# Optimization experiments

Hardware: AMD Instinct MI355X
Metric: run time of the kernel (lower is better)

The kernel has to match this reference:

```python
import jax, jax.numpy as jnp
import numpy as np

V = 32000   # vocab_size
S = 4096    # seq_len
D = 1024    # dim
H = 4096    # hidden_dim
L = 2       # num_layers
CS = 64     # chunk_size
R = 256     # low_rank_dim = max(8, D//4)
WIN = 8     # window_size (OptitationLayer default)
NEG = -1e30


def setup_inputs() -> dict:
    key = jax.random.key(0)
    ks = jax.random.split(key, 20)
    f32 = jnp.float32
    inp = {}
    inp['idx_seq'] = jax.random.randint(ks[0], (S,), 0, V)
    inp['embeddings'] = jax.random.normal(ks[1], (V, D), f32) * 0.01
    inp['positional'] = jax.random.normal(ks[2], (S, D), f32) * 0.01
    # per-layer MLP params, stacked over layer axis
    inp['Wg'] = jax.random.normal(ks[3], (L, D, D), f32) / D ** 0.5
    inp['bg'] = jnp.zeros((L, D), f32)
    inp['Ws'] = jax.random.normal(ks[4], (L, D, H), f32) / D ** 0.5
    inp['bs'] = jnp.zeros((L, H), f32)
    inp['Wo'] = jax.random.normal(ks[5], (L, H, D), f32) / H ** 0.5
    inp['bo'] = jnp.zeros((L, D), f32)
    # per-layer optitation (windowed attention) params
    inp['Wq'] = jax.random.normal(ks[6], (L, D, R), f32) / D ** 0.5
    inp['Wk'] = jax.random.normal(ks[7], (L, D, R), f32) / D ** 0.5
    inp['Wv'] = jax.random.normal(ks[8], (L, D, R), f32) / D ** 0.5
    inp['Wao'] = jax.random.normal(ks[9], (L, R, D), f32) / R ** 0.5
    inp['bq'] = jnp.zeros((L, R), f32)
    inp['bk'] = jnp.zeros((L, R), f32)
    inp['bv'] = jnp.zeros((L, R), f32)
    inp['bao'] = jnp.zeros((L, D), f32)
    inp['outW'] = jax.random.normal(ks[10], (D, V), f32) / D ** 0.5
    inp['outb'] = jnp.zeros((V,), f32)
    return inp


def _optitation(x, Wq, bq, Wk, bk, Wv, bv, Wao, bao):
    Q = x @ Wq + bq
    K = x @ Wk + bk
    Vv = x @ Wv + bv
    s = x.shape[0]
    off = jnp.arange(WIN + 1)
    j = jnp.arange(s)[:, None] - off[None, :]  # [s, w+1] key indices
    valid = j >= 0
    jc = jnp.maximum(j, 0)
    Kw = K[jc]   # [s, w+1, R]
    Vw = Vv[jc]  # [s, w+1, R]
    scores = jnp.einsum('sr,swr->sw', Q, Kw) / jnp.sqrt(jnp.float32(R))
    scores = jnp.where(valid, scores, NEG)
    attn = jax.nn.softmax(scores, axis=-1)
    ao = jnp.einsum('sw,swr->sr', attn, Vw)   # [s, R]
    return ao @ Wao + bao


def _chunk_link(x):
    # chunk-averaging with half-weighted neighbor chunks
    s, d = x.shape
    pad = (-s) % CS
    xp = jnp.pad(x, ((0, pad), (0, 0)))
    n = xp.shape[0] // CS
    c = xp.reshape(n, CS, d)
    prev = jnp.concatenate([jnp.zeros_like(c[:1]), c[:-1]], axis=0)
    nxt = jnp.concatenate([c[1:], jnp.zeros_like(c[:1])], axis=0)
    i = jnp.arange(n)
    w = 1.0 + 0.5 * (i > 0).astype(x.dtype) + 0.5 * (i < n - 1).astype(x.dtype)
    upd = (c + 0.5 * prev + 0.5 * nxt) / w[:, None, None]
    return upd.reshape(-1, d)[:s]


def reference(idx_seq, embeddings, positional, Wg, bg, Ws, bs, Wo, bo,
              Wq, bq, Wk, bk, Wv, bv, Wao, bao, outW, outb):
    s = idx_seq.shape[0]
    x = embeddings[idx_seq] + positional[:s]
    # decay accumulation: x[pos] += 0.8**pos * x[0] for pos >= 1 (x[0] untouched)
    decay = jnp.power(jnp.float32(0.8), jnp.arange(s, dtype=jnp.float32))
    decay = decay.at[0].set(0.0)
    x = x + decay[:, None] * x[0]
    for l in range(L):
        residual = x
        x = x * jax.nn.sigmoid(x @ Wg[l] + bg[l])            # lensed gate
        x = jnp.tanh(x @ Ws[l] + bs[l]) @ Wo[l] + bo[l]       # context sculpt
        x = x + residual
        x = x + _optitation(x, Wq[l], bq[l], Wk[l], bk[l],
                            Wv[l], bv[l], Wao[l], bao[l])
        x = _chunk_link(x)
    return x @ outW + outb
```

## Files before the change

### kernel.cpp

```cpp
#include <hip/hip_runtime.h>
#include <hip/hip_bf16.h>
#include <math.h>

#define S_LEN 4096
#define DIM   1024
#define HID   4096
#define NLAYER 2
#define RDIM  256
#define VOCAB 32000
#define QKVN  768

typedef unsigned short u16;
typedef __attribute__((ext_vector_type(8))) short s16x8;
typedef __attribute__((ext_vector_type(4))) float f32x4;
typedef __attribute__((ext_vector_type(4))) unsigned short u16x4;

__device__ inline u16 f2b(float f){
  unsigned u = __float_as_uint(f);
  u += 0x7fff + ((u >> 16) & 1);
  return (u16)(u >> 16);
}

__device__ inline void gload_lds16(const void* g, void* l){
  __builtin_amdgcn_global_load_lds((__attribute__((address_space(1))) void*)(g),
                                   (__attribute__((address_space(3))) void*)(l), 16, 0, 0);
}

__global__ void k_transpose(const float* __restrict__ src, u16* __restrict__ dst,
                            int K, int N, size_t srcLS, size_t dstLS){
  __shared__ float tile[32][33];
  src += (size_t)blockIdx.z * srcLS;
  dst += (size_t)blockIdx.z * dstLS;
  int n0 = blockIdx.x * 32, k0 = blockIdx.y * 32;
  int tx = threadIdx.x, ty = threadIdx.y;
  #pragma unroll
  for (int i = 0; i < 32; i += 8)
    tile[ty + i][tx] = src[(size_t)(k0 + ty + i) * N + n0 + tx];
  __syncthreads();
  #pragma unroll
  for (int i = 0; i < 32; i += 8)
    dst[(size_t)(n0 + ty + i) * K + k0 + tx] = f2b(tile[tx][ty + i]);
}

__global__ void k_embed(const int* __restrict__ idx, const float* __restrict__ emb,
                        const float* __restrict__ pos, float* __restrict__ xf,
                        u16* __restrict__ xb){
  int s = blockIdx.x;
  int d = blockIdx.y * 256 + threadIdx.x;
  float v = emb[(size_t)idx[s] * DIM + d] + pos[(size_t)s * DIM + d];
  if (s > 0){
    float x0 = emb[(size_t)idx[0] * DIM + d] + pos[d];
    v += exp2f((float)s * -0.3219280948873623f) * x0;
  }
  size_t o = (size_t)s * DIM + d;
  xf[o] = v; xb[o] = f2b(v);
}

#define EP_GATE  0
#define EP_TANH  1
#define EP_RESID 2
#define EP_BIASF 3
#define EP_AO    4
#define EP_OUT   5

#define PH_SYNC() do{ asm volatile("" ::: "memory"); __builtin_amdgcn_s_barrier(); asm volatile("" ::: "memory"); }while(0)


#define MMA_QUAD(MH, NLO, BF) \
  { _Pragma("unroll") for (int mi = 0; mi < 4; mi++){ \
    _Pragma("unroll") for (int ni = 0; ni < 2; ni++){ \
      _Pragma("unroll") for (int ks = 0; ks < 2; ks++){ \
        acc[(MH)*4+mi][(NLO)+ni] = __builtin_amdgcn_mfma_f32_16x16x32_bf16((BF)[ni*2+ks], af[mi*2+ks], acc[(MH)*4+mi][(NLO)+ni], 0, 0, 0); } } } }

#define LDA(MH, BO) \
  { _Pragma("unroll") for (int mi = 0; mi < 4; mi++){ \
    _Pragma("unroll") for (int ks = 0; ks < 2; ks++){ \
      af[mi*2+ks] = *(const s16x8*)(pa0 + (BO) + ((MH)*4+mi)*1024 + ((ks ^ kb) * 32)); } } }

#define LDB(NH, BO) \
  { _Pragma("unroll") for (int ni = 0; ni < 2; ni++){ \
    _Pragma("unroll") for (int ks = 0; ks < 2; ks++){ \
      bf_[(NH)*4+ni*2+ks] = *(const s16x8*)(pb0 + (BO) + ((NH)*2+ni)*1024 + ((ks ^ kb) * 32)); } } }

template<int EPI>
__global__ __launch_bounds__(512, 2) void k_gemm8(
    const u16* __restrict__ A, const u16* __restrict__ Bt,
    const float* __restrict__ bias,
    float* __restrict__ outf, u16* __restrict__ outbf,
    int N, int K, int tilesM, int tilesN){
  extern __shared__ u16 lds[];
  const int t = threadIdx.x;
  const int w = t >> 6, l = t & 63;
  const int wr = w >> 2, wc = w & 3;
  const int NT = K >> 6;
  const int NI = NT >> 1;

  int nwg = tilesM * tilesN;
  int id = blockIdx.x, id2;
  if ((nwg & 7) == 0){ int c = nwg >> 3; id2 = (id & 7) * c + (id >> 3); }
  else id2 = id;
  int per = tilesM << 3;
  int g = id2 / per, r = id2 % per;
  int bm = r % tilesM;
  int bn = (g << 3) + r / tilesM;
  const int bRow = bm * 256, bCol = bn * 256;

  const int r0 = t >> 3;
  const int scol = (((t & 7) ^ ((t >> 3) & 7)) * 8);

  auto stage_half = [&](int tau, int q){
    if (tau >= NT) return;
    int h = q & 1;
    bool isA = q < 2;
    const u16* gp = (isA ? A + (size_t)bRow * K : Bt + (size_t)bCol * K)
                 + (size_t)(h * 128 + r0) * K + (size_t)tau * 64 + scol;
    u16* d = lds + (isA ? 0 : 32768) + ((tau & 1) * 16384) + h * 8192 + t * 8;
    gload_lds16(gp, d);
    gload_lds16(gp + (size_t)64 * K, d + 4096);
  };

  const int cb = (((l >> 4) ^ (l & 3)) * 8);
  const int kb = (l >> 2) & 1;
  const u16* pa0 = lds + (wr * 128 + (l & 15)) * 64 + cb;
  const u16* pb0 = lds + 32768 + (wc * 64 + (l & 15)) * 64 + cb;

  f32x4 acc[8][4] = {};
  s16x8 af[8], bf_[8];

  stage_half(0, 0); stage_half(0, 1); stage_half(0, 2); stage_half(0, 3);
  stage_half(1, 0);
  asm volatile("s_waitcnt vmcnt(2)" ::: "memory");
  PH_SYNC();

  for (int i = 0; i < NI; i++){
    const int t1 = 2 * i + 1, t2 = 2 * i + 2, t3 = 2 * i + 3;
    const bool last = (i + 1 == NI);
    LDA(0, 0); LDB(0, 0);
    stage_half(t1, 1);
    PH_SYNC();
    __builtin_amdgcn_s_setprio(1); MMA_QUAD(0, 0, bf_); __builtin_amdgcn_s_setprio(0);
    PH_SYNC();
    LDB(1, 0);
    stage_half(t1, 2);
    PH_SYNC();
    __builtin_amdgcn_s_setprio(1); MMA_QUAD(0, 2, bf_ + 4); __builtin_amdgcn_s_setprio(0);
    PH_SYNC();
    LDA(1, 0);
    stage_half(t1, 3);
    PH_SYNC();
    __builtin_amdgcn_s_setprio(1); MMA_QUAD(1, 2, bf_ + 4); __builtin_amdgcn_s_setprio(0);
    PH_SYNC();
    stage_half(t2, 0);
    if (!last) asm volatile("s_waitcnt vmcnt(2)" ::: "memory");
    else       asm volatile("s_waitcnt vmcnt(0)" ::: "memory");
    PH_SYNC();
    __builtin_amdgcn_s_setprio(1); MMA_QUAD(1, 0, bf_); __builtin_amdgcn_s_setprio(0);
    PH_SYNC();
    LDA(0, 16384); LDB(0, 16384);
    stage_half(t2, 1);
    PH_SYNC();
    __builtin_amdgcn_s_setprio(1); MMA_QUAD(0, 0, bf_); __builtin_amdgcn_s_setprio(0);
    PH_SYNC();
    LDB(1, 16384);
    stage_half(t2, 2);
    PH_SYNC();
    __builtin_amdgcn_s_setprio(1); MMA_QUAD(0, 2, bf_ + 4); __builtin_amdgcn_s_setprio(0);
    PH_SYNC();
    LDA(1, 16384);
    stage_half(t2, 3);
    PH_SYNC();
    __builtin_amdgcn_s_setprio(1); MMA_QUAD(1, 2, bf_ + 4); __builtin_amdgcn_s_setprio(0);
    PH_SYNC();
    stage_half(t3, 0);
    if (!last) asm volatile("s_waitcnt vmcnt(2)" ::: "memory");
    PH_SYNC();
    __builtin_amdgcn_s_setprio(1); MMA_QUAD(1, 0, bf_); __builtin_amdgcn_s_setprio(0);
    PH_SYNC();
  }

  #pragma unroll
  for (int m = 0; m < 8; m++){
    int gr = bRow + wr * 128 + m * 16 + (l & 15);
    #pragma unroll
    for (int n = 0; n < 4; n++){
      int gc = bCol + wc * 64 + n * 16 + ((l >> 4) * 4);
      f32x4 v = acc[m][n] + *(const f32x4*)(bias + gc);
      *(f32x4*)(outf + (size_t)gr * N + gc) = v;
    }
  }
}


#define MMA2(MH, NL) \
  { _Pragma("unroll") for (int mi = 0; mi < 2; mi++){ \
    _Pragma("unroll") for (int ks = 0; ks < 2; ks++){ \
      acc[(MH)*2+mi][(NL)] = __builtin_amdgcn_mfma_f32_16x16x32_bf16(bf_[(NL)*2+ks], af[mi*2+ks], acc[(MH)*2+mi][(NL)], 0, 0, 0); } } }

#define LDA2(MH, BO) \
  { _Pragma("unroll") for (int mi = 0; mi < 2; mi++){ \
    _Pragma("unroll") for (int ks = 0; ks < 2; ks++){ \
      af[mi*2+ks] = *(const s16x8*)(pa0 + (BO) + ((MH)*2+mi)*1024 + ((ks ^ kb) * 32)); } } }

#define LDB2(NL, BO) \
  { _Pragma("unroll") for (int ks = 0; ks < 2; ks++){ \
    bf_[(NL)*2+ks] = *(const s16x8*)(pb0 + (BO) + (NL)*1024 + ((ks ^ kb) * 32)); } }

template<int EPI>
__global__ __launch_bounds__(512, 4) void k_gemm8b(
    const u16* __restrict__ A, const u16* __restrict__ Bt,
    const float* __restrict__ bias, const float* __restrict__ aux,
    float* __restrict__ outf, u16* __restrict__ outbf,
    int N, int K, int tilesM, int tilesN){
  extern __shared__ u16 lds[];
  const int t = threadIdx.x;
  const int w = t >> 6, l = t & 63;
  const int wr = w >> 2, wc = w & 3;
  const int NT = K >> 6;
  const int NI = NT >> 1;

  int nwg = tilesM * tilesN;
  int id = blockIdx.x, id2;
  if ((nwg & 7) == 0){ int c = nwg >> 3; id2 = (id & 7) * c + (id >> 3); }
  else id2 = id;
  int bm = id2 % tilesM, bn = id2 / tilesM;
  const int bRow = bm * 128, bCol = bn * 128;

  const int r0 = t >> 3;
  const int scol = (((t & 7) ^ ((t >> 3) & 7)) * 8);

  auto stage_half = [&](int tau, int q){
    if (tau >= NT) return;
    int h = q & 1;
    bool isA = q < 2;
    const u16* gp = (isA ? A + (size_t)bRow * K : Bt + (size_t)bCol * K)
                 + (size_t)(h * 64 + r0) * K + (size_t)tau * 64 + scol;
    u16* d = lds + (isA ? 0 : 16384) + ((tau & 1) * 8192) + h * 4096 + t * 8;
    gload_lds16(gp, d);
  };

  const int cb = (((l >> 4) ^ (l & 3)) * 8);
  const int kb = (l >> 2) & 1;
  const u16* pa0 = lds + wr * 4096 + (l & 15) * 64 + cb;
  const u16* pb0 = lds + 16384 + (wc >> 1) * 4096 + ((wc & 1) * 32 + (l & 15)) * 64 + cb;

  f32x4 acc[4][2] = {};
  s16x8 af[4], bf_[4];

  stage_half(0, 0); stage_half(0, 1); stage_half(0, 2); stage_half(0, 3);
  stage_half(1, 0);
  asm volatile("s_waitcnt vmcnt(1)" ::: "memory");
  PH_SYNC();

  for (int i = 0; i < NI; i++){
    const int t1 = 2 * i + 1, t2 = 2 * i + 2, t3 = 2 * i + 3;
    const bool last = (i + 1 == NI);
    LDA2(0, 0); LDB2(0, 0);
    stage_half(t1, 1);
    PH_SYNC();
    __builtin_amdgcn_s_setprio(1); MMA2(0, 0); __builtin_amdgcn_s_setprio(0);
    PH_SYNC();
    LDB2(1, 0);
    stage_half(t1, 2);
    PH_SYNC();
    __builtin_amdgcn_s_setprio(1); MMA2(0, 1); __builtin_amdgcn_s_setprio(0);
    PH_SYNC();
    LDA2(1, 0);
    stage_half(t1, 3);
    PH_SYNC();
    __builtin_amdgcn_s_setprio(1); MMA2(1, 1); __builtin_amdgcn_s_setprio(0);
    PH_SYNC();
    stage_half(t2, 0);
    if (!last) asm volatile("s_waitcnt vmcnt(1)" ::: "memory");
    else       asm volatile("s_waitcnt vmcnt(0)" ::: "memory");
    PH_SYNC();
    __builtin_amdgcn_s_setprio(1); MMA2(1, 0); __builtin_amdgcn_s_setprio(0);
    PH_SYNC();
    LDA2(0, 8192); LDB2(0, 8192);
    stage_half(t2, 1);
    PH_SYNC();
    __builtin_amdgcn_s_setprio(1); MMA2(0, 0); __builtin_amdgcn_s_setprio(0);
    PH_SYNC();
    LDB2(1, 8192);
    stage_half(t2, 2);
    PH_SYNC();
    __builtin_amdgcn_s_setprio(1); MMA2(0, 1); __builtin_amdgcn_s_setprio(0);
    PH_SYNC();
    LDA2(1, 8192);
    stage_half(t2, 3);
    PH_SYNC();
    __builtin_amdgcn_s_setprio(1); MMA2(1, 1); __builtin_amdgcn_s_setprio(0);
    PH_SYNC();
    stage_half(t3, 0);
    if (!last) asm volatile("s_waitcnt vmcnt(1)" ::: "memory");
    PH_SYNC();
    __builtin_amdgcn_s_setprio(1); MMA2(1, 0); __builtin_amdgcn_s_setprio(0);
    PH_SYNC();
  }

  #pragma unroll
  for (int m = 0; m < 4; m++){
    int gr = bRow + wr * 64 + m * 16 + (l & 15);
    #pragma unroll
    for (int n = 0; n < 2; n++){
      int gc = bCol + wc * 32 + n * 16 + ((l >> 4) * 4);
      size_t o = (size_t)gr * N + gc;
      f32x4 v = acc[m][n] + *(const f32x4*)(bias + gc);
      if constexpr (EPI == EP_GATE){
        f32x4 a = *(const f32x4*)(aux + o);
        u16x4 rr;
        #pragma unroll
        for (int q = 0; q < 4; q++) rr[q] = f2b(a[q] / (1.f + expf(-v[q])));
        *(u16x4*)(outbf + o) = rr;
      } else if constexpr (EPI == EP_TANH){
        u16x4 rr;
        #pragma unroll
        for (int q = 0; q < 4; q++) rr[q] = f2b(tanhf(v[q]));
        *(u16x4*)(outbf + o) = rr;
      } else if constexpr (EPI == EP_RESID){
        v += *(const f32x4*)(aux + o);
        *(f32x4*)(outf + o) = v;
        u16x4 rr;
        #pragma unroll
        for (int q = 0; q < 4; q++) rr[q] = f2b(v[q]);
        *(u16x4*)(outbf + o) = rr;
      } else if constexpr (EPI == EP_BIASF){
        *(f32x4*)(outf + o) = v;
      } else if constexpr (EPI == EP_AO){
        v += *(const f32x4*)(aux + o);
        *(f32x4*)(outf + o) = v;
      } else {
        *(f32x4*)(outf + o) = v;
      }
    }
  }
}

__global__ void k_attn(const float* __restrict__ qkv, u16* __restrict__ aob){
  int s = blockIdx.x;
  int l = threadIdx.x;
  const float* qp = qkv + (size_t)s * QKVN;
  float qr[4];
  #pragma unroll
  for (int r = 0; r < 4; r++) qr[r] = qp[l + 64 * r];
  float sc[9];
  float mx = -1e30f;
  #pragma unroll
  for (int j = 0; j <= 8; j++){
    int sj = s - j;
    bool ok = sj >= 0;
    int row = ok ? sj : 0;
    const float* kp = qkv + (size_t)row * QKVN + RDIM;
    float p = 0.f;
    #pragma unroll
    for (int r = 0; r < 4; r++) p += qr[r] * kp[l + 64 * r];
    #pragma unroll
    for (int off = 32; off; off >>= 1) p += __shfl_xor(p, off);
    p = ok ? p * 0.0625f : -1e30f;
    sc[j] = p;
    mx = fmaxf(mx, p);
  }
  float den = 0.f;
  #pragma unroll
  for (int j = 0; j <= 8; j++){ sc[j] = expf(sc[j] - mx); den += sc[j]; }
  float inv = 1.f / den;
  #pragma unroll
  for (int r = 0; r < 4; r++){
    float a = 0.f;
    #pragma unroll
    for (int j = 0; j <= 8; j++){
      int sj = s - j;
      int row = sj >= 0 ? sj : 0;
      a += sc[j] * qkv[(size_t)row * QKVN + 512 + l + 64 * r];
    }
    aob[(size_t)s * RDIM + l + 64 * r] = f2b(a * inv);
  }
}

__global__ void k_chunk(const float* __restrict__ xin, float* __restrict__ xout,
                        u16* __restrict__ xb){
  int s = blockIdx.x;
  int d = blockIdx.y * 256 + threadIdx.x;
  int ci = s >> 6;
  float v = xin[(size_t)s * DIM + d];
  float wsum = 1.f;
  if (ci > 0){ v += 0.5f * xin[(size_t)(s - 64) * DIM + d]; wsum += 0.5f; }
  if (ci < 63){ v += 0.5f * xin[(size_t)(s + 64) * DIM + d]; wsum += 0.5f; }
  v /= wsum;
  size_t o = (size_t)s * DIM + d;
  xout[o] = v; xb[o] = f2b(v);
}

__global__ void k_concat3(const float* __restrict__ a, const float* __restrict__ b,
                          const float* __restrict__ c, float* __restrict__ dst){
  int i = threadIdx.x;
  dst[i] = a[i]; dst[256 + i] = b[i]; dst[512 + i] = c[i];
}

extern "C" void kernel_launch(void* const* d_in, const int* in_sizes, int n_in,
                              void* d_out, int out_size, void* d_ws, size_t ws_size,
                              hipStream_t stream){
  const int*   idx  = (const int*)d_in[0];
  const float* emb  = (const float*)d_in[1];
  const float* pos  = (const float*)d_in[2];
  const float* Wg   = (const float*)d_in[3];
  const float* bg   = (const float*)d_in[4];
  const float* Ws_  = (const float*)d_in[5];
  const float* bs   = (const float*)d_in[6];
  const float* Wo   = (const float*)d_in[7];
  const float* bo   = (const float*)d_in[8];
  const float* Wq   = (const float*)d_in[9];
  const float* Wk   = (const float*)d_in[10];
  const float* Wv   = (const float*)d_in[11];
  const float* Wao  = (const float*)d_in[12];
  const float* bq   = (const float*)d_in[13];
  const float* bk   = (const float*)d_in[14];
  const float* bv   = (const float*)d_in[15];
  const float* bao  = (const float*)d_in[16];
  const float* outW = (const float*)d_in[17];
  const float* outb = (const float*)d_in[18];
  float* out = (float*)d_out;

  char* p = (char*)d_ws;
  auto alloc = [&](size_t n)->char*{ char* r = p; p += (n + 255) & ~(size_t)255; return r; };
  float* xfA  = (float*)alloc((size_t)S_LEN * DIM * 4);
  float* xfB  = (float*)alloc((size_t)S_LEN * DIM * 4);
  u16*   xb   = (u16*)  alloc((size_t)S_LEN * DIM * 2);
  u16*   xgb  = (u16*)  alloc((size_t)S_LEN * DIM * 2);
  u16*   tbuf = (u16*)  alloc((size_t)S_LEN * HID * 2);
  float* qkvf = (float*)alloc((size_t)S_LEN * QKVN * 4);
  u16*   aob  = (u16*)  alloc((size_t)S_LEN * RDIM * 2);
  float* bqkv = (float*)alloc(QKVN * 4);
  u16*   WgT  = (u16*)  alloc((size_t)NLAYER * DIM * DIM * 2);
  u16*   WsT  = (u16*)  alloc((size_t)NLAYER * DIM * HID * 2);
  u16*   WoT  = (u16*)  alloc((size_t)NLAYER * HID * DIM * 2);
  u16*   WqkvT= (u16*)  alloc((size_t)NLAYER * QKVN * DIM * 2);
  u16*   WaoT = (u16*)  alloc((size_t)NLAYER * RDIM * DIM * 2);
  u16*   outWT= (u16*)  alloc((size_t)VOCAB * DIM * 2);

  hipFuncSetAttribute((const void*)&k_gemm8<EP_OUT>,
                      hipFuncAttributeMaxDynamicSharedMemorySize, 131072);
  hipFuncSetAttribute((const void*)&k_gemm8b<EP_GATE>,
                      hipFuncAttributeMaxDynamicSharedMemorySize, 65536);
  hipFuncSetAttribute((const void*)&k_gemm8b<EP_TANH>,
                      hipFuncAttributeMaxDynamicSharedMemorySize, 65536);
  hipFuncSetAttribute((const void*)&k_gemm8b<EP_RESID>,
                      hipFuncAttributeMaxDynamicSharedMemorySize, 65536);
  hipFuncSetAttribute((const void*)&k_gemm8b<EP_BIASF>,
                      hipFuncAttributeMaxDynamicSharedMemorySize, 65536);
  hipFuncSetAttribute((const void*)&k_gemm8b<EP_AO>,
                      hipFuncAttributeMaxDynamicSharedMemorySize, 65536);

  dim3 tb32(32, 8);
  k_transpose<<<dim3(DIM/32,  DIM/32,  NLAYER), tb32, 0, stream>>>(Wg,  WgT,  DIM, DIM,  (size_t)DIM*DIM,  (size_t)DIM*DIM);
  k_transpose<<<dim3(HID/32,  DIM/32,  NLAYER), tb32, 0, stream>>>(Ws_, WsT,  DIM, HID,  (size_t)DIM*HID,  (size_t)DIM*HID);
  k_transpose<<<dim3(DIM/32,  HID/32,  NLAYER), tb32, 0, stream>>>(Wo,  WoT,  HID, DIM,  (size_t)HID*DIM,  (size_t)HID*DIM);
  k_transpose<<<dim3(RDIM/32, DIM/32,  NLAYER), tb32, 0, stream>>>(Wq,  WqkvT,                 DIM, RDIM, (size_t)DIM*RDIM, (size_t)QKVN*DIM);
  k_transpose<<<dim3(RDIM/32, DIM/32,  NLAYER), tb32, 0, stream>>>(Wk,  WqkvT + (size_t)256*DIM, DIM, RDIM, (size_t)DIM*RDIM, (size_t)QKVN*DIM);
  k_transpose<<<dim3(RDIM/32, DIM/32,  NLAYER), tb32, 0, stream>>>(Wv,  WqkvT + (size_t)512*DIM, DIM, RDIM, (size_t)DIM*RDIM, (size_t)QKVN*DIM);
  k_transpose<<<dim3(DIM/32,  RDIM/32, NLAYER), tb32, 0, stream>>>(Wao, WaoT, RDIM, DIM, (size_t)RDIM*DIM, (size_t)RDIM*DIM);
  k_transpose<<<dim3(VOCAB/32, DIM/32, 1),      tb32, 0, stream>>>(outW, outWT, DIM, VOCAB, 0, 0);

  k_embed<<<dim3(S_LEN, DIM/256), 256, 0, stream>>>(idx, emb, pos, xfA, xb);

  float* curF = xfA; float* altF = xfB;
  for (int l = 0; l < NLAYER; l++){
    k_gemm8b<EP_GATE ><<<(S_LEN/128)*(DIM/128),  512, 65536, stream>>>(xb,  WgT  + (size_t)l*DIM*DIM,  bg + (size_t)l*DIM, curF, nullptr, xgb, DIM, DIM, S_LEN/128, DIM/128);
    k_gemm8b<EP_TANH ><<<(S_LEN/128)*(HID/128),  512, 65536, stream>>>(xgb, WsT  + (size_t)l*DIM*HID,  bs + (size_t)l*HID, nullptr, nullptr, tbuf, HID, DIM, S_LEN/128, HID/128);
    k_gemm8b<EP_RESID><<<(S_LEN/128)*(DIM/128),  512, 65536, stream>>>(tbuf,WoT  + (size_t)l*HID*DIM,  bo + (size_t)l*DIM, curF, curF, xb, DIM, HID, S_LEN/128, DIM/128);
    k_concat3<<<1, 256, 0, stream>>>(bq + (size_t)l*RDIM, bk + (size_t)l*RDIM, bv + (size_t)l*RDIM, bqkv);
    k_gemm8b<EP_BIASF><<<(S_LEN/128)*(QKVN/128), 512, 65536, stream>>>(xb,  WqkvT + (size_t)l*QKVN*DIM, bqkv, nullptr, qkvf, nullptr, QKVN, DIM, S_LEN/128, QKVN/128);
    k_attn<<<S_LEN, 64, 0, stream>>>(qkvf, aob);
    k_gemm8b<EP_AO   ><<<(S_LEN/128)*(DIM/128),  512, 65536, stream>>>(aob, WaoT + (size_t)l*RDIM*DIM, bao + (size_t)l*DIM, curF, curF, nullptr, DIM, RDIM, S_LEN/128, DIM/128);
    k_chunk<<<dim3(S_LEN, DIM/256), 256, 0, stream>>>(curF, altF, xb);
    float* tmp = curF; curF = altF; altF = tmp;
  }
  k_gemm8<EP_OUT><<<(S_LEN/256)*(VOCAB/256), 512, 131072, stream>>>(xb, outWT, outb, out, nullptr, VOCAB, DIM, S_LEN/256, VOCAB/256);
}
```

Measured before the change: 909.8 us.

## Vectorize weight transpose, retile GEMM block order, batch attention rows per block

The weight transpose now works on 64x64 tiles, reading with float4 loads and writing four bf16 values per store, to cut the number of memory transactions in the per-call weight conversion. The large output GEMM changes its block-to-tile mapping to pairs of M tiles walking across N, and the 128-tile GEMM switches to grouped-by-8 column ordering, both to improve L2 reuse. The attention kernel packs four sequence rows into one 256-thread block to reduce launch and scheduling overhead for tiny blocks. The transpose's 64x65 float tile has column reads with stride 65, which may cause some LDS bank conflicts.

```diff
diff --git a/kernel.cpp b/kernel.cpp
--- a/kernel.cpp
+++ b/kernel.cpp
@@ -28,18 +28,27 @@
 
 __global__ void k_transpose(const float* __restrict__ src, u16* __restrict__ dst,
                             int K, int N, size_t srcLS, size_t dstLS){
-  __shared__ float tile[32][33];
+  __shared__ float tile[64][65];
   src += (size_t)blockIdx.z * srcLS;
   dst += (size_t)blockIdx.z * dstLS;
-  int n0 = blockIdx.x * 32, k0 = blockIdx.y * 32;
+  int n0 = blockIdx.x * 64, k0 = blockIdx.y * 64;
   int tx = threadIdx.x, ty = threadIdx.y;
   #pragma unroll
-  for (int i = 0; i < 32; i += 8)
-    tile[ty + i][tx] = src[(size_t)(k0 + ty + i) * N + n0 + tx];
+  for (int i = 0; i < 4; i++){
+    float4 v = *(const float4*)&src[(size_t)(k0 + ty + 16 * i) * N + n0 + tx * 4];
+    tile[ty + 16 * i][tx * 4 + 0] = v.x;
+    tile[ty + 16 * i][tx * 4 + 1] = v.y;
+    tile[ty + 16 * i][tx * 4 + 2] = v.z;
+    tile[ty + 16 * i][tx * 4 + 3] = v.w;
+  }
   __syncthreads();
   #pragma unroll
-  for (int i = 0; i < 32; i += 8)
-    dst[(size_t)(n0 + ty + i) * K + k0 + tx] = f2b(tile[tx][ty + i]);
+  for (int i = 0; i < 4; i++){
+    u16x4 o;
+    #pragma unroll
+    for (int j = 0; j < 4; j++) o[j] = f2b(tile[tx * 4 + j][ty + 16 * i]);
+    *(u16x4*)&dst[(size_t)(n0 + ty + 16 * i) * K + k0 + tx * 4] = o;
+  }
 }
 
 __global__ void k_embed(const int* __restrict__ idx, const float* __restrict__ emb,
@@ -99,10 +108,10 @@
   int id = blockIdx.x, id2;
   if ((nwg & 7) == 0){ int c = nwg >> 3; id2 = (id & 7) * c + (id >> 3); }
   else id2 = id;
-  int per = tilesM << 3;
-  int g = id2 / per, r = id2 % per;
-  int bm = r % tilesM;
-  int bn = (g << 3) + r / tilesM;
+  int pr = tilesN * 2;
+  int stripe = id2 / pr, r2 = id2 % pr;
+  int bm = stripe * 2 + (r2 & 1);
+  int bn = r2 >> 1;
   const int bRow = bm * 256, bCol = bn * 256;
 
   const int r0 = t >> 3;
@@ -222,7 +231,10 @@
   int id = blockIdx.x, id2;
   if ((nwg & 7) == 0){ int c = nwg >> 3; id2 = (id & 7) * c + (id >> 3); }
   else id2 = id;
-  int bm = id2 % tilesM, bn = id2 / tilesM;
+  int per = tilesM << 3;
+  int g = id2 / per, r = id2 % per;
+  int bm = r % tilesM;
+  int bn = (g << 3) + r / tilesM;
   const int bRow = bm * 128, bCol = bn * 128;
 
   const int r0 = t >> 3;
@@ -336,8 +348,8 @@
 }
 
 __global__ void k_attn(const float* __restrict__ qkv, u16* __restrict__ aob){
-  int s = blockIdx.x;
-  int l = threadIdx.x;
+  int s = blockIdx.x * 4 + (threadIdx.x >> 6);
+  int l = threadIdx.x & 63;
   const float* qp = qkv + (size_t)s * QKVN;
   float qr[4];
   #pragma unroll
@@ -437,28 +449,28 @@
   u16*   WaoT = (u16*)  alloc((size_t)NLAYER * RDIM * DIM * 2);
   u16*   outWT= (u16*)  alloc((size_t)VOCAB * DIM * 2);
 
-  hipFuncSetAttribute((const void*)&k_gemm8<EP_OUT>,
+  (void)hipFuncSetAttribute((const void*)&k_gemm8<EP_OUT>,
                       hipFuncAttributeMaxDynamicSharedMemorySize, 131072);
-  hipFuncSetAttribute((const void*)&k_gemm8b<EP_GATE>,
+  (void)hipFuncSetAttribute((const void*)&k_gemm8b<EP_GATE>,
                       hipFuncAttributeMaxDynamicSharedMemorySize, 65536);
-  hipFuncSetAttribute((const void*)&k_gemm8b<EP_TANH>,
+  (void)hipFuncSetAttribute((const void*)&k_gemm8b<EP_TANH>,
                       hipFuncAttributeMaxDynamicSharedMemorySize, 65536);
-  hipFuncSetAttribute((const void*)&k_gemm8b<EP_RESID>,
+  (void)hipFuncSetAttribute((const void*)&k_gemm8b<EP_RESID>,
                       hipFuncAttributeMaxDynamicSharedMemorySize, 65536);
-  hipFuncSetAttribute((const void*)&k_gemm8b<EP_BIASF>,
+  (void)hipFuncSetAttribute((const void*)&k_gemm8b<EP_BIASF>,
                       hipFuncAttributeMaxDynamicSharedMemorySize, 65536);
-  hipFuncSetAttribute((const void*)&k_gemm8b<EP_AO>,
+  (void)hipFuncSetAttribute((const void*)&k_gemm8b<EP_AO>,
                       hipFuncAttributeMaxDynamicSharedMemorySize, 65536);
 
-  dim3 tb32(32, 8);
-  k_transpose<<<dim3(DIM/32,  DIM/32,  NLAYER), tb32, 0, stream>>>(Wg,  WgT,  DIM, DIM,  (size_t)DIM*DIM,  (size_t)DIM*DIM);
-  k_transpose<<<dim3(HID/32,  DIM/32,  NLAYER), tb32, 0, stream>>>(Ws_, WsT,  DIM, HID,  (size_t)DIM*HID,  (size_t)DIM*HID);
-  k_transpose<<<dim3(DIM/32,  HID/32,  NLAYER), tb32, 0, stream>>>(Wo,  WoT,  HID, DIM,  (size_t)HID*DIM,  (size_t)HID*DIM);
-  k_transpose<<<dim3(RDIM/32, DIM/32,  NLAYER), tb32, 0, stream>>>(Wq,  WqkvT,                 DIM, RDIM, (size_t)DIM*RDIM, (size_t)QKVN*DIM);
-  k_transpose<<<dim3(RDIM/32, DIM/32,  NLAYER), tb32, 0, stream>>>(Wk,  WqkvT + (size_t)256*DIM, DIM, RDIM, (size_t)DIM*RDIM, (size_t)QKVN*DIM);
-  k_transpose<<<dim3(RDIM/32, DIM/32,  NLAYER), tb32, 0, stream>>>(Wv,  WqkvT + (size_t)512*DIM, DIM, RDIM, (size_t)DIM*RDIM, (size_t)QKVN*DIM);
-  k_transpose<<<dim3(DIM/32,  RDIM/32, NLAYER), tb32, 0, stream>>>(Wao, WaoT, RDIM, DIM, (size_t)RDIM*DIM, (size_t)RDIM*DIM);
-  k_transpose<<<dim3(VOCAB/32, DIM/32, 1),      tb32, 0, stream>>>(outW, outWT, DIM, VOCAB, 0, 0);
+  dim3 tb16(16, 16);
+  k_transpose<<<dim3(DIM/64,  DIM/64,  NLAYER), tb16, 0, stream>>>(Wg,  WgT,  DIM, DIM,  (size_t)DIM*DIM,  (size_t)DIM*DIM);
+  k_transpose<<<dim3(HID/64,  DIM/64,  NLAYER), tb16, 0, stream>>>(Ws_, WsT,  DIM, HID,  (size_t)DIM*HID,  (size_t)DIM*HID);
+  k_transpose<<<dim3(DIM/64,  HID/64,  NLAYER), tb16, 0, stream>>>(Wo,  WoT,  HID, DIM,  (size_t)HID*DIM,  (size_t)HID*DIM);
+  k_transpose<<<dim3(RDIM/64, DIM/64,  NLAYER), tb16, 0, stream>>>(Wq,  WqkvT,                 DIM, RDIM, (size_t)DIM*RDIM, (size_t)QKVN*DIM);
+  k_transpose<<<dim3(RDIM/64, DIM/64,  NLAYER), tb16, 0, stream>>>(Wk,  WqkvT + (size_t)256*DIM, DIM, RDIM, (size_t)DIM*RDIM, (size_t)QKVN*DIM);
+  k_transpose<<<dim3(RDIM/64, DIM/64,  NLAYER), tb16, 0, stream>>>(Wv,  WqkvT + (size_t)512*DIM, DIM, RDIM, (size_t)DIM*RDIM, (size_t)QKVN*DIM);
+  k_transpose<<<dim3(DIM/64,  RDIM/64, NLAYER), tb16, 0, stream>>>(Wao, WaoT, RDIM, DIM, (size_t)RDIM*DIM, (size_t)RDIM*DIM);
+  k_transpose<<<dim3(VOCAB/64, DIM/64, 1),      tb16, 0, stream>>>(outW, outWT, DIM, VOCAB, 0, 0);
 
   k_embed<<<dim3(S_LEN, DIM/256), 256, 0, stream>>>(idx, emb, pos, xfA, xb);
 
@@ -469,7 +481,7 @@
     k_gemm8b<EP_RESID><<<(S_LEN/128)*(DIM/128),  512, 65536, stream>>>(tbuf,WoT  + (size_t)l*HID*DIM,  bo + (size_t)l*DIM, curF, curF, xb, DIM, HID, S_LEN/128, DIM/128);
     k_concat3<<<1, 256, 0, stream>>>(bq + (size_t)l*RDIM, bk + (size_t)l*RDIM, bv + (size_t)l*RDIM, bqkv);
     k_gemm8b<EP_BIASF><<<(S_LEN/128)*(QKVN/128), 512, 65536, stream>>>(xb,  WqkvT + (size_t)l*QKVN*DIM, bqkv, nullptr, qkvf, nullptr, QKVN, DIM, S_LEN/128, QKVN/128);
-    k_attn<<<S_LEN, 64, 0, stream>>>(qkvf, aob);
+    k_attn<<<S_LEN/4, 256, 0, stream>>>(qkvf, aob);
     k_gemm8b<EP_AO   ><<<(S_LEN/128)*(DIM/128),  512, 65536, stream>>>(aob, WaoT + (size_t)l*RDIM*DIM, bao + (size_t)l*DIM, curF, curF, nullptr, DIM, RDIM, S_LEN/128, DIM/128);
     k_chunk<<<dim3(S_LEN, DIM/256), 256, 0, stream>>>(curF, altF, xb);
     float* tmp = curF; curF = altF; altF = tmp;
```

Measured after the change: 884.6 us. 2.8% less time.
